# Kernel optimization log

Measured on AMD Instinct MI355X. Metric: run time of the kernel, lower is better.

## Reference

```python
import jax, jax.numpy as jnp
import numpy as np

D_MODEL = 1024
NUM_HEADS = 16
D_K = D_MODEL // NUM_HEADS


def setup_inputs() -> dict:
    key = jax.random.key(0)
    ks = jax.random.split(key, 9)
    s = 1.0 / np.sqrt(D_MODEL)
    x = jax.random.normal(ks[0], (2, 2048, D_MODEL), dtype=jnp.float32)
    mk = lambda k: jax.random.uniform(k, (D_MODEL, D_MODEL), jnp.float32, -s, s)
    mb = lambda k: jax.random.uniform(k, (D_MODEL,), jnp.float32, -s, s)
    return {
        "x": x,
        "Wq": mk(ks[1]), "bq": mb(ks[2]),
        "Wk": mk(ks[3]), "bk": mb(ks[4]),
        "Wv": mk(ks[5]), "bv": mb(ks[6]),
        "Wo": mk(ks[7]), "bo": mb(ks[8]),
    }


def _attn(x, Wq, bq, Wk, bk, Wv, bv, Wo, bo):
    B, S, _ = x.shape
    # torch Linear: y = x @ W.T + b; weights stored [out, in]
    def proj(W, b):
        y = jnp.einsum('bsd,ed->bse', x, W) + b
        return y.reshape(B, S, NUM_HEADS, D_K).transpose(0, 2, 1, 3)  # [B,H,S,Dk]
    Q = proj(Wq, bq)
    K = proj(Wk, bk)
    V = proj(Wv, bv)
    scale = 1.0 / np.sqrt(D_K).astype(np.float32)
    scores = jnp.einsum('bhqd,bhkd->bhqk', Q, K) * scale  # [B,H,S,S]
    # FAITHFUL to source: softmax over dim=1 (the HEAD axis), a quirk of the original code
    attn = jax.nn.softmax(scores, axis=1)
    context = jnp.einsum('bhqk,bhkd->bhqd', attn, V)  # [B,H,S,Dk]
    context = context.transpose(0, 2, 1, 3).reshape(B, S, D_MODEL)
    return jnp.einsum('bsd,ed->bse', context, Wo) + bo


def reference(x, Wq, bq, Wk, bk, Wv, bv, Wo, bo):
    return _attn(x, Wq, bq, Wk, bk, Wv, bv, Wo, bo)
```

## Files before the change

kernel.cpp:

```cpp
#include <hip/hip_runtime.h>


#define D_MODEL 1024
#define NH 16
#define DKH 64
#define SEQ 2048
#define NB 2
#define NTOK (NB * SEQ)
#define OSC 0.180336880f

typedef float f32x4 __attribute__((ext_vector_type(4)));
typedef short bf16x8 __attribute__((ext_vector_type(8)));

static __device__ __forceinline__ unsigned short f2bf(float x) {
    union { float f; unsigned int u; } c; c.f = x;
    unsigned int r = (c.u + 0x7FFFu + ((c.u >> 16) & 1u)) >> 16;
    return (unsigned short)r;
}
static __device__ __forceinline__ unsigned int pack2(float a, float b) {
    return (unsigned int)f2bf(a) | ((unsigned int)f2bf(b) << 16);
}
static __device__ __forceinline__ unsigned int pack2rn(float a, float b) {
    union { float f; unsigned int u; } ca, cb; ca.f = a; cb.f = b;
    return __builtin_amdgcn_perm(cb.u + 0x8000u, ca.u + 0x8000u, 0x07060302u);
}
static __device__ __forceinline__ unsigned int pack2tr(float a, float b) {
    union { float f; unsigned int u; } ca, cb; ca.f = a; cb.f = b;
    return __builtin_amdgcn_perm(cb.u, ca.u, 0x07060302u);
}
static __device__ __forceinline__ float bflo(unsigned int u) {
    union { unsigned int x; float f; } c; c.x = u << 16; return c.f;
}
static __device__ __forceinline__ float bfhi(unsigned int u) {
    union { unsigned int x; float f; } c; c.x = u & 0xFFFF0000u; return c.f;
}
static __device__ __forceinline__ f32x4 mfma16(uint4 a, uint4 b, f32x4 c) {
    return __builtin_amdgcn_mfma_f32_16x16x32_bf16(
        __builtin_bit_cast(bf16x8, a), __builtin_bit_cast(bf16x8, b), c, 0, 0, 0);
}
static __device__ __forceinline__ void gl_lds16(const unsigned short* g, unsigned short* l) {
    __builtin_amdgcn_global_load_lds(
        (const __attribute__((address_space(1))) unsigned int*)g,
        (__attribute__((address_space(3))) unsigned int*)l, 16, 0, 0);
}
static __device__ __forceinline__ int fsw(int row) {
    return (row & 7) ^ ((row >> 2) & 7);
}

__global__ __launch_bounds__(256) void cvt_k(const float* __restrict__ x,
                                             unsigned short* __restrict__ xb)
{
    size_t i = ((size_t)blockIdx.x * 256 + threadIdx.x) * 8;
    float4 a = *(const float4*)(x + i);
    float4 b = *(const float4*)(x + i + 4);
    uint4 p = { pack2(a.x, a.y), pack2(a.z, a.w), pack2(b.x, b.y), pack2(b.z, b.w) };
    *(uint4*)(xb + i) = p;
}

__global__ __launch_bounds__(256) void cvt_w3(
    const float* __restrict__ w0, const float* __restrict__ w1,
    const float* __restrict__ w2, unsigned short* __restrict__ outb)
{
    int sel = blockIdx.x >> 9;
    int blk = blockIdx.x & 511;
    const float* src = (sel == 0) ? w0 : (sel == 1) ? w1 : w2;
    size_t i = ((size_t)blk * 256 + threadIdx.x) * 8;
    float4 a = *(const float4*)(src + i);
    float4 b = *(const float4*)(src + i + 4);
    uint4 p = { pack2(a.x, a.y), pack2(a.z, a.w), pack2(b.x, b.y), pack2(b.z, b.w) };
    *(uint4*)(outb + (size_t)sel * D_MODEL * D_MODEL + i) = p;
}

__global__ __launch_bounds__(256) void gemm_qkv3(
    const unsigned short* __restrict__ A, const unsigned short* __restrict__ Wb3,
    const float* __restrict__ bq, const float* __restrict__ bk,
    const float* __restrict__ bv, unsigned short* __restrict__ Qh,
    unsigned short* __restrict__ Kh, unsigned short* __restrict__ Vt)
{
    __shared__ unsigned short lds[16384];
    unsigned short* lA = lds;
    unsigned short* lB = lds + 8192;
    const int tid = threadIdx.x;
    const int wv = tid >> 6, lane = tid & 63, quad = lane >> 4, lm = lane & 15;
    const int sel = blockIdx.x >> 3;
    const int m0 = blockIdx.y * 128, n0 = (blockIdx.x & 7) * 128;
    const int sub = lane >> 3, chl = (lane & 7) ^ sub;
    const unsigned short* Wb = Wb3 + (size_t)sel * D_MODEL * D_MODEL;
    const float* bias = (sel == 0) ? bq : (sel == 1) ? bk : bv;
    const float osc = (sel == 0) ? OSC : 1.0f;

    f32x4 acc[2][8] = {};

    for (int k0 = 0; k0 < D_MODEL; k0 += 64) {
        __syncthreads();
#pragma unroll
        for (int j = 0; j < 4; ++j) {
            int rbase = wv * 32 + j * 8;
            gl_lds16(A + (size_t)(m0 + rbase + sub) * D_MODEL + k0 + chl * 8,
                     &lA[rbase * 64]);
            gl_lds16(Wb + (size_t)(n0 + rbase + sub) * D_MODEL + k0 + chl * 8,
                     &lB[rbase * 64]);
        }
        __syncthreads();
#pragma unroll
        for (int ks = 0; ks < 2; ++ks) {
            uint4 af[2];
#pragma unroll
            for (int mt = 0; mt < 2; ++mt)
                af[mt] = *(const uint4*)&lA[(wv * 32 + mt * 16 + lm) * 64 +
                                            ((ks * 4 + quad) ^ (lm & 7)) * 8];
#pragma unroll
            for (int nt = 0; nt < 8; ++nt) {
                uint4 bf = *(const uint4*)&lB[(nt * 16 + lm) * 64 +
                                              ((ks * 4 + quad) ^ (lm & 7)) * 8];
                acc[0][nt] = mfma16(af[0], bf, acc[0][nt]);
                acc[1][nt] = mfma16(af[1], bf, acc[1][nt]);
            }
        }
    }

    if (sel < 2) {
        unsigned short* out = (sel == 0) ? Qh : Kh;
#pragma unroll
        for (int nt = 0; nt < 8; ++nt) {
            int n = n0 + nt * 16 + lm;
            float bvv = bias[n];
            int h = n >> 6, d = n & 63;
#pragma unroll
            for (int mt = 0; mt < 2; ++mt)
#pragma unroll
                for (int r = 0; r < 4; ++r) {
                    int m = m0 + wv * 32 + mt * 16 + quad * 4 + r;
                    int b = m >> 11, q = m & 2047;
                    out[((size_t)(b * NH + h) * SEQ + q) * DKH + d] =
                        f2bf((acc[mt][nt][r] + bvv) * osc);
                }
        }
    } else {
        __syncthreads();
        unsigned short* T = lds;
#pragma unroll
        for (int nt = 0; nt < 8; ++nt) {
            float bvv = bias[n0 + nt * 16 + lm];
            int nl = nt * 16 + lm;
#pragma unroll
            for (int mt = 0; mt < 2; ++mt) {
                int ml = wv * 32 + mt * 16 + quad * 4;
                uint2 p = { pack2rn(acc[mt][nt][0] + bvv, acc[mt][nt][1] + bvv),
                            pack2rn(acc[mt][nt][2] + bvv, acc[mt][nt][3] + bvv) };
                *(uint2*)&T[nl * 128 + ml] = p;
            }
        }
        __syncthreads();
        int row = tid >> 1, seg = tid & 1;
        int b = m0 >> 11, s0 = m0 & 2047;
        unsigned short* dst = Vt + ((size_t)(b * D_MODEL) + n0 + row) * SEQ + s0 + seg * 64;
        const unsigned short* src = &T[row * 128 + seg * 64];
#pragma unroll
        for (int i = 0; i < 8; ++i)
            *(uint4*)(dst + i * 8) = *(const uint4*)(src + i * 8);
    }
}

template <int KS>
__global__ __launch_bounds__(256) void psum(const unsigned short* __restrict__ OP,
                                            unsigned short* __restrict__ OPs)
{
    const size_t M = (size_t)NTOK * D_MODEL;
    size_t i = ((size_t)blockIdx.x * 256 + threadIdx.x) * 8;
    uint4 a = *(const uint4*)(OP + i);
    float lo0 = bflo(a.x), hi0 = bfhi(a.x), lo1 = bflo(a.y), hi1 = bfhi(a.y);
    float lo2 = bflo(a.z), hi2 = bfhi(a.z), lo3 = bflo(a.w), hi3 = bfhi(a.w);
#pragma unroll
    for (int p = 1; p < KS; ++p) {
        uint4 u = *(const uint4*)(OP + p * M + i);
        lo0 += bflo(u.x); hi0 += bfhi(u.x); lo1 += bflo(u.y); hi1 += bfhi(u.y);
        lo2 += bflo(u.z); hi2 += bfhi(u.z); lo3 += bflo(u.w); hi3 += bfhi(u.w);
    }
    uint4 o = { pack2(lo0, hi0), pack2(lo1, hi1), pack2(lo2, hi2), pack2(lo3, hi3) };
    *(uint4*)(OPs + i) = o;
}

__global__ __launch_bounds__(256) void gemm_osum1(
    const unsigned short* __restrict__ OPs, const unsigned short* __restrict__ WoB,
    const float* __restrict__ bias, float* __restrict__ out)
{
    __shared__ unsigned short lds[16384];
    unsigned short* lA = lds;
    unsigned short* lB = lds + 8192;
    const int tid = threadIdx.x;
    const int wv = tid >> 6, lane = tid & 63, quad = lane >> 4, lm = lane & 15;
    const int m0 = blockIdx.y * 128, n0 = blockIdx.x * 128;
    const int sub = lane >> 3, chl = (lane & 7) ^ sub;
    const int b = m0 >> 11, q0 = m0 & 2047;

    f32x4 acc[2][8] = {};

    for (int k0 = 0; k0 < D_MODEL; k0 += 64) {
        const int h = k0 >> 6;
        const unsigned short* Ab = OPs + ((size_t)(b * NH + h) * SEQ + q0) * DKH;
        __syncthreads();
#pragma unroll
        for (int j = 0; j < 4; ++j) {
            int rbase = wv * 32 + j * 8;
            gl_lds16(Ab + (size_t)(rbase + sub) * DKH + chl * 8, &lA[rbase * 64]);
            gl_lds16(WoB + (size_t)(n0 + rbase + sub) * D_MODEL + k0 + chl * 8,
                     &lB[rbase * 64]);
        }
        __syncthreads();
#pragma unroll
        for (int ks = 0; ks < 2; ++ks) {
            uint4 af[2];
#pragma unroll
            for (int mt = 0; mt < 2; ++mt)
                af[mt] = *(const uint4*)&lA[(wv * 32 + mt * 16 + lm) * 64 +
                                            ((ks * 4 + quad) ^ (lm & 7)) * 8];
#pragma unroll
            for (int nt = 0; nt < 8; ++nt) {
                uint4 bf = *(const uint4*)&lB[(nt * 16 + lm) * 64 +
                                              ((ks * 4 + quad) ^ (lm & 7)) * 8];
                acc[0][nt] = mfma16(af[0], bf, acc[0][nt]);
                acc[1][nt] = mfma16(af[1], bf, acc[1][nt]);
            }
        }
    }
#pragma unroll
    for (int nt = 0; nt < 8; ++nt) {
        int n = n0 + nt * 16 + lm;
        float bv = bias[n];
#pragma unroll
        for (int mt = 0; mt < 2; ++mt)
#pragma unroll
            for (int r = 0; r < 4; ++r) {
                int m = m0 + wv * 32 + mt * 16 + quad * 4 + r;
                out[(size_t)m * D_MODEL + n] = acc[mt][nt][r] + bv;
            }
    }
}

__global__ __launch_bounds__(256) void zker2(
    const unsigned short* __restrict__ Qh, const unsigned short* __restrict__ Kh,
    unsigned short* __restrict__ rz)
{
    __shared__ unsigned short lK[2][128 * 64];
    const int tid = threadIdx.x;
    const int wv = tid >> 6, lane = tid & 63, quad = lane >> 4, lm = lane & 15;
    const int lid = blockIdx.x;
    const int xcd = lid & 7, slot = lid >> 3;
    const int qb = slot & 15, col = xcd * 4 + (slot >> 4);
    const int b = col >> 4, kb = col & 15;
    const int q0 = qb * 128, k0 = kb * 128;
    const int srow = tid >> 3, sc = tid & 7;

    f32x4 z[2][8] = {};

    auto stagek = [&](int buf, int hh) {
        const size_t kbase = ((size_t)(b * NH + hh) * SEQ + k0) * DKH;
#pragma unroll
        for (int j = 0; j < 4; ++j) {
            int row = j * 32 + srow;
            int g = sc ^ fsw(row);
            gl_lds16(Kh + kbase + (size_t)row * 64 + g * 8,
                     &lK[buf][(j * 32 + wv * 8) * 64]);
        }
    };
    auto loadq = [&](uint4 (&bqr)[2][2], int hh) {
#pragma unroll
        for (int qs = 0; qs < 2; ++qs) {
            const unsigned short* qp = Qh +
                ((size_t)(b * NH + hh) * SEQ + q0 + wv * 32 + qs * 16 + lm) * DKH + quad * 8;
            bqr[qs][0] = *(const uint4*)qp;
            bqr[qs][1] = *(const uint4*)(qp + 32);
        }
    };

    uint4 bq[2][2];
    stagek(0, 0);
    loadq(bq, 0);
    __syncthreads();

    for (int h = 0; h < NH; ++h) {
        const int cur = h & 1;
        uint4 bqn[2][2];
        if (h + 1 < NH) {
            stagek(cur ^ 1, h + 1);
            loadq(bqn, h + 1);
        }
        const unsigned short* cK = lK[cur];
#pragma unroll
        for (int kt = 0; kt < 8; ++kt) {
            int krow = kt * 16 + lm;
            uint4 a0 = *(const uint4*)&cK[krow * 64 + ((quad) ^ fsw(krow)) * 8];
            uint4 a1 = *(const uint4*)&cK[krow * 64 + ((4 + quad) ^ fsw(krow)) * 8];
#pragma unroll
            for (int qs = 0; qs < 2; ++qs) {
                f32x4 sf = {0.f, 0.f, 0.f, 0.f};
                __builtin_amdgcn_s_setprio(1);
                sf = mfma16(a0, bq[qs][0], sf);
                sf = mfma16(a1, bq[qs][1], sf);
                __builtin_amdgcn_s_setprio(0);
#pragma unroll
                for (int r = 0; r < 4; ++r)
                    z[qs][kt][r] += __builtin_amdgcn_exp2f(sf[r]);
            }
        }
        __syncthreads();
        if (h + 1 < NH) {
#pragma unroll
            for (int qs = 0; qs < 2; ++qs) {
                bq[qs][0] = bqn[qs][0];
                bq[qs][1] = bqn[qs][1];
            }
        }
    }
#pragma unroll
    for (int qs = 0; qs < 2; ++qs) {
        int q = q0 + wv * 32 + qs * 16 + lm;
#pragma unroll
        for (int kt = 0; kt < 8; ++kt) {
            int k = k0 + kt * 16 + quad * 4;
            float l0 = __builtin_amdgcn_logf(z[qs][kt][0]);
            float l1 = __builtin_amdgcn_logf(z[qs][kt][1]);
            float l2 = __builtin_amdgcn_logf(z[qs][kt][2]);
            float l3 = __builtin_amdgcn_logf(z[qs][kt][3]);
            uint2 st = { pack2rn(-l0, -l1), pack2rn(-l2, -l3) };
            *(uint2*)(rz + (size_t)(b * SEQ + q) * SEQ + k) = st;
        }
    }
}

template <int KS>
__global__ __launch_bounds__(256) void attn4(
    const unsigned short* __restrict__ Qh, const unsigned short* __restrict__ Kh,
    const unsigned short* __restrict__ Vt, const unsigned short* __restrict__ rz,
    unsigned short* __restrict__ OP)
{
    __shared__ unsigned short lK[2][64 * 64];
    __shared__ unsigned short lV[2][64 * 64];
    const int tid = threadIdx.x;
    const int wv = tid >> 6, lane = tid & 63, quad = lane >> 4, lm = lane & 15;
    const int lid = blockIdx.x;
    const int xcd = lid & 7, slot = lid >> 3;
    const int qb = slot & 15;
    const int combo = xcd * (4 * KS) + (slot >> 4);
    const int bh = combo / KS, ksl = combo % KS;
    const int b = bh >> 4, h = bh & 15;
    const int q0 = qb * 128;
    const int NIT = (SEQ / KS) / 64;
    const int kbeg = ksl * (SEQ / KS);
    const int q0w = q0 + wv * 32;
    const size_t hb = (size_t)(b * NH + h) * SEQ;
    const int srow = tid >> 3, sc = tid & 7;

    uint4 qf[2][2];
#pragma unroll
    for (int qs = 0; qs < 2; ++qs)
#pragma unroll
        for (int ks = 0; ks < 2; ++ks)
            qf[qs][ks] = *(const uint4*)(Qh + (hb + q0w + qs * 16 + lm) * DKH +
                                         ks * 32 + quad * 8);

    auto stage = [&](int buf, int kb2) {
#pragma unroll
        for (int j = 0; j < 2; ++j) {
            int row = j * 32 + srow;
            int g = sc ^ fsw(row);
            gl_lds16(Kh + (hb + kb2 + row) * DKH + g * 8,
                     &lK[buf][(j * 32 + wv * 8) * 64]);
        }
#pragma unroll
        for (int j = 0; j < 2; ++j) {
            int row = j * 32 + srow;
            int g = sc ^ fsw(row);
            gl_lds16(Vt + ((size_t)(b * D_MODEL) + h * DKH + row) * SEQ + kb2 + g * 8,
                     &lV[buf][(j * 32 + wv * 8) * 64]);
        }
    };
    auto loadrv = [&](uint4 (&r)[2][2], int kb2) {
#pragma unroll
        for (int qs = 0; qs < 2; ++qs)
#pragma unroll
            for (int gr = 0; gr < 2; ++gr)
                r[gr][qs] = *(const uint4*)(rz +
                    (size_t)(b * SEQ + q0w + qs * 16 + lm) * SEQ +
                    kb2 + gr * 32 + quad * 8);
    };

    const int perm = ((lm >> 2) * 8) + (lm & 3);
    f32x4 oa[4][2] = {};

    uint4 rv[2][2];
    stage(0, kbeg);
    loadrv(rv, kbeg);
    __syncthreads();

    for (int kt = 0; kt < NIT; ++kt) {
        const int cur = kt & 1;
        const int kbase = kbeg + kt * 64;
        uint4 rvn[2][2];
        if (kt + 1 < NIT) {
            stage(cur ^ 1, kbase + 64);
            loadrv(rvn, kbase + 64);
        }
        const unsigned short* cK = lK[cur];
        const unsigned short* cV = lV[cur];

#pragma unroll
        for (int gr = 0; gr < 2; ++gr) {
            f32x4 sf[2][2];
#pragma unroll
            for (int qs = 0; qs < 2; ++qs) {
                uint4 rq = rv[gr][qs];
                sf[0][qs][0] = bflo(rq.x); sf[0][qs][1] = bfhi(rq.x);
                sf[0][qs][2] = bflo(rq.y); sf[0][qs][3] = bfhi(rq.y);
                sf[1][qs][0] = bflo(rq.z); sf[1][qs][1] = bfhi(rq.z);
                sf[1][qs][2] = bflo(rq.w); sf[1][qs][3] = bfhi(rq.w);
            }
            __builtin_amdgcn_s_setprio(1);
#pragma unroll
            for (int sel = 0; sel < 2; ++sel) {
                int key = gr * 32 + perm + sel * 4;
#pragma unroll
                for (int ks = 0; ks < 2; ++ks) {
                    uint4 kfv = *(const uint4*)&cK[key * 64 +
                                                   ((ks * 4 + quad) ^ fsw(key)) * 8];
                    sf[sel][0] = mfma16(kfv, qf[0][ks], sf[sel][0]);
                    sf[sel][1] = mfma16(kfv, qf[1][ks], sf[sel][1]);
                }
            }
            __builtin_amdgcn_s_setprio(0);
            uint4 pk[2];
#pragma unroll
            for (int qs = 0; qs < 2; ++qs) {
                float p00 = __builtin_amdgcn_exp2f(sf[0][qs][0]);
                float p01 = __builtin_amdgcn_exp2f(sf[0][qs][1]);
                float p02 = __builtin_amdgcn_exp2f(sf[0][qs][2]);
                float p03 = __builtin_amdgcn_exp2f(sf[0][qs][3]);
                float p10 = __builtin_amdgcn_exp2f(sf[1][qs][0]);
                float p11 = __builtin_amdgcn_exp2f(sf[1][qs][1]);
                float p12 = __builtin_amdgcn_exp2f(sf[1][qs][2]);
                float p13 = __builtin_amdgcn_exp2f(sf[1][qs][3]);
                pk[qs].x = pack2tr(p00, p01);
                pk[qs].y = pack2tr(p02, p03);
                pk[qs].z = pack2tr(p10, p11);
                pk[qs].w = pack2tr(p12, p13);
            }
            __builtin_amdgcn_s_setprio(1);
#pragma unroll
            for (int ct = 0; ct < 4; ++ct) {
                int vrow = ct * 16 + lm;
                uint4 vfv = *(const uint4*)&cV[vrow * 64 +
                                               ((gr * 4 + quad) ^ fsw(vrow)) * 8];
                oa[ct][0] = mfma16(vfv, pk[0], oa[ct][0]);
                oa[ct][1] = mfma16(vfv, pk[1], oa[ct][1]);
            }
            __builtin_amdgcn_s_setprio(0);
        }
        __syncthreads();
        if (kt + 1 < NIT) {
#pragma unroll
            for (int a = 0; a < 2; ++a)
#pragma unroll
                for (int c = 0; c < 2; ++c)
                    rv[a][c] = rvn[a][c];
        }
    }

    unsigned short* op = OP + (size_t)ksl * NTOK * D_MODEL;
#pragma unroll
    for (int ct = 0; ct < 4; ++ct)
#pragma unroll
        for (int qs = 0; qs < 2; ++qs) {
            uint2 st = { pack2rn(oa[ct][qs][0], oa[ct][qs][1]),
                         pack2rn(oa[ct][qs][2], oa[ct][qs][3]) };
            *(uint2*)(op + (hb + q0w + qs * 16 + lm) * DKH + ct * 16 + quad * 4) = st;
        }
}

extern "C" void kernel_launch(void* const* d_in, const int* in_sizes, int n_in,
                              void* d_out, int out_size, void* d_ws, size_t ws_size,
                              hipStream_t stream)
{
    const float* x  = (const float*)d_in[0];
    const float* Wq = (const float*)d_in[1];
    const float* bq = (const float*)d_in[2];
    const float* Wk = (const float*)d_in[3];
    const float* bk = (const float*)d_in[4];
    const float* Wv = (const float*)d_in[5];
    const float* bv = (const float*)d_in[6];
    const float* Wo = (const float*)d_in[7];
    const float* bo = (const float*)d_in[8];
    float* out = (float*)d_out;

    const size_t M  = (size_t)NTOK * D_MODEL;
    const size_t RZ = (size_t)NB * SEQ * SEQ;
    unsigned short* ws = (unsigned short*)d_ws;
    unsigned short* rzb = ws;
    unsigned short* xb  = ws;
    unsigned short* Qh  = ws + RZ;
    unsigned short* Kh  = Qh + M;
    unsigned short* Vt  = Kh + M;
    unsigned short* OP  = Vt + M;
    unsigned short* Wb3 = OP;
    unsigned short* OPs = Qh;
    unsigned short* WoB = rzb;

    const size_t need4 = (RZ + 3 * M + 4 * M) * sizeof(unsigned short);
    const size_t need2 = (RZ + 3 * M + 2 * M) * sizeof(unsigned short);
    const int KS = (ws_size >= need4) ? 4 : (ws_size >= need2) ? 2 : 1;

    cvt_k<<<2048, 256, 0, stream>>>(x, xb);
    cvt_w3<<<1536, 256, 0, stream>>>(Wq, Wk, Wv, Wb3);
    gemm_qkv3<<<dim3(24, 32), 256, 0, stream>>>(xb, Wb3, bq, bk, bv, Qh, Kh, Vt);
    zker2<<<512, 256, 0, stream>>>(Qh, Kh, rzb);
    if (KS == 4)      attn4<4><<<2048, 256, 0, stream>>>(Qh, Kh, Vt, rzb, OP);
    else if (KS == 2) attn4<2><<<1024, 256, 0, stream>>>(Qh, Kh, Vt, rzb, OP);
    else              attn4<1><<<512, 256, 0, stream>>>(Qh, Kh, Vt, rzb, OP);
    cvt_k<<<512, 256, 0, stream>>>(Wo, WoB);
    if (KS == 4)      psum<4><<<2048, 256, 0, stream>>>(OP, OPs);
    else if (KS == 2) psum<2><<<2048, 256, 0, stream>>>(OP, OPs);
    else              OPs = OP;
    gemm_osum1<<<dim3(8, 32), 256, 0, stream>>>(OPs, WoB, bo, out);
}
```

Measured before the change: 272.2 us.

## Shrink output GEMM tile to 128x64 and drop attention double-buffering

```diff
diff --git a/kernel.cpp b/kernel.cpp
--- a/kernel.cpp
+++ b/kernel.cpp
@@ -181,20 +181,21 @@
     *(uint4*)(OPs + i) = o;
 }
 
-__global__ __launch_bounds__(256) void gemm_osum1(
+__global__ __launch_bounds__(256) void gemm_osum2(
     const unsigned short* __restrict__ OPs, const unsigned short* __restrict__ WoB,
     const float* __restrict__ bias, float* __restrict__ out)
 {
-    __shared__ unsigned short lds[16384];
+    __shared__ unsigned short lds[12288];
     unsigned short* lA = lds;
     unsigned short* lB = lds + 8192;
     const int tid = threadIdx.x;
     const int wv = tid >> 6, lane = tid & 63, quad = lane >> 4, lm = lane & 15;
-    const int m0 = blockIdx.y * 128, n0 = blockIdx.x * 128;
+    const int wm = wv >> 1, wn = wv & 1;
+    const int m0 = blockIdx.y * 128, n0 = blockIdx.x * 64;
     const int sub = lane >> 3, chl = (lane & 7) ^ sub;
     const int b = m0 >> 11, q0 = m0 & 2047;
 
-    f32x4 acc[2][8] = {};
+    f32x4 acc[4][2] = {};
 
     for (int k0 = 0; k0 < D_MODEL; k0 += 64) {
         const int h = k0 >> 6;
@@ -204,35 +205,40 @@
         for (int j = 0; j < 4; ++j) {
             int rbase = wv * 32 + j * 8;
             gl_lds16(Ab + (size_t)(rbase + sub) * DKH + chl * 8, &lA[rbase * 64]);
+        }
+#pragma unroll
+        for (int j = 0; j < 2; ++j) {
+            int rbase = wv * 16 + j * 8;
             gl_lds16(WoB + (size_t)(n0 + rbase + sub) * D_MODEL + k0 + chl * 8,
                      &lB[rbase * 64]);
         }
         __syncthreads();
 #pragma unroll
         for (int ks = 0; ks < 2; ++ks) {
-            uint4 af[2];
-#pragma unroll
-            for (int mt = 0; mt < 2; ++mt)
-                af[mt] = *(const uint4*)&lA[(wv * 32 + mt * 16 + lm) * 64 +
+            uint4 af[4];
+#pragma unroll
+            for (int mt = 0; mt < 4; ++mt)
+                af[mt] = *(const uint4*)&lA[(wm * 64 + mt * 16 + lm) * 64 +
                                             ((ks * 4 + quad) ^ (lm & 7)) * 8];
 #pragma unroll
-            for (int nt = 0; nt < 8; ++nt) {
-                uint4 bf = *(const uint4*)&lB[(nt * 16 + lm) * 64 +
+            for (int nt = 0; nt < 2; ++nt) {
+                uint4 bf = *(const uint4*)&lB[(wn * 32 + nt * 16 + lm) * 64 +
                                               ((ks * 4 + quad) ^ (lm & 7)) * 8];
-                acc[0][nt] = mfma16(af[0], bf, acc[0][nt]);
-                acc[1][nt] = mfma16(af[1], bf, acc[1][nt]);
-            }
-        }
-    }
-#pragma unroll
-    for (int nt = 0; nt < 8; ++nt) {
-        int n = n0 + nt * 16 + lm;
+#pragma unroll
+                for (int mt = 0; mt < 4; ++mt)
+                    acc[mt][nt] = mfma16(af[mt], bf, acc[mt][nt]);
+            }
+        }
+    }
+#pragma unroll
+    for (int nt = 0; nt < 2; ++nt) {
+        int n = n0 + wn * 32 + nt * 16 + lm;
         float bv = bias[n];
 #pragma unroll
-        for (int mt = 0; mt < 2; ++mt)
+        for (int mt = 0; mt < 4; ++mt)
 #pragma unroll
             for (int r = 0; r < 4; ++r) {
-                int m = m0 + wv * 32 + mt * 16 + quad * 4 + r;
+                int m = m0 + wm * 64 + mt * 16 + quad * 4 + r;
                 out[(size_t)m * D_MODEL + n] = acc[mt][nt][r] + bv;
             }
     }
@@ -335,8 +341,8 @@
     const unsigned short* __restrict__ Vt, const unsigned short* __restrict__ rz,
     unsigned short* __restrict__ OP)
 {
-    __shared__ unsigned short lK[2][64 * 64];
-    __shared__ unsigned short lV[2][64 * 64];
+    __shared__ unsigned short lK[64 * 64];
+    __shared__ unsigned short lV[64 * 64];
     const int tid = threadIdx.x;
     const int wv = tid >> 6, lane = tid & 63, quad = lane >> 4, lm = lane & 15;
     const int lid = blockIdx.x;
@@ -360,50 +366,35 @@
             qf[qs][ks] = *(const uint4*)(Qh + (hb + q0w + qs * 16 + lm) * DKH +
                                          ks * 32 + quad * 8);
 
-    auto stage = [&](int buf, int kb2) {
+    const int perm = ((lm >> 2) * 8) + (lm & 3);
+    f32x4 oa[4][2] = {};
+
+    for (int kt = 0; kt < NIT; ++kt) {
+        const int kbase = kbeg + kt * 64;
+        __syncthreads();
 #pragma unroll
         for (int j = 0; j < 2; ++j) {
             int row = j * 32 + srow;
             int g = sc ^ fsw(row);
-            gl_lds16(Kh + (hb + kb2 + row) * DKH + g * 8,
-                     &lK[buf][(j * 32 + wv * 8) * 64]);
+            gl_lds16(Kh + (hb + kbase + row) * DKH + g * 8,
+                     &lK[(j * 32 + wv * 8) * 64]);
         }
 #pragma unroll
         for (int j = 0; j < 2; ++j) {
             int row = j * 32 + srow;
             int g = sc ^ fsw(row);
-            gl_lds16(Vt + ((size_t)(b * D_MODEL) + h * DKH + row) * SEQ + kb2 + g * 8,
-                     &lV[buf][(j * 32 + wv * 8) * 64]);
-        }
-    };
-    auto loadrv = [&](uint4 (&r)[2][2], int kb2) {
+            gl_lds16(Vt + ((size_t)(b * D_MODEL) + h * DKH + row) * SEQ + kbase + g * 8,
+                     &lV[(j * 32 + wv * 8) * 64]);
+        }
+        uint4 rv[2][2];
 #pragma unroll
         for (int qs = 0; qs < 2; ++qs)
 #pragma unroll
             for (int gr = 0; gr < 2; ++gr)
-                r[gr][qs] = *(const uint4*)(rz +
+                rv[gr][qs] = *(const uint4*)(rz +
                     (size_t)(b * SEQ + q0w + qs * 16 + lm) * SEQ +
-                    kb2 + gr * 32 + quad * 8);
-    };
-
-    const int perm = ((lm >> 2) * 8) + (lm & 3);
-    f32x4 oa[4][2] = {};
-
-    uint4 rv[2][2];
-    stage(0, kbeg);
-    loadrv(rv, kbeg);
-    __syncthreads();
-
-    for (int kt = 0; kt < NIT; ++kt) {
-        const int cur = kt & 1;
-        const int kbase = kbeg + kt * 64;
-        uint4 rvn[2][2];
-        if (kt + 1 < NIT) {
-            stage(cur ^ 1, kbase + 64);
-            loadrv(rvn, kbase + 64);
-        }
-        const unsigned short* cK = lK[cur];
-        const unsigned short* cV = lV[cur];
+                    kbase + gr * 32 + quad * 8);
+        __syncthreads();
 
 #pragma unroll
         for (int gr = 0; gr < 2; ++gr) {
@@ -422,7 +413,7 @@
                 int key = gr * 32 + perm + sel * 4;
 #pragma unroll
                 for (int ks = 0; ks < 2; ++ks) {
-                    uint4 kfv = *(const uint4*)&cK[key * 64 +
+                    uint4 kfv = *(const uint4*)&lK[key * 64 +
                                                    ((ks * 4 + quad) ^ fsw(key)) * 8];
                     sf[sel][0] = mfma16(kfv, qf[0][ks], sf[sel][0]);
                     sf[sel][1] = mfma16(kfv, qf[1][ks], sf[sel][1]);
@@ -449,20 +440,12 @@
 #pragma unroll
             for (int ct = 0; ct < 4; ++ct) {
                 int vrow = ct * 16 + lm;
-                uint4 vfv = *(const uint4*)&cV[vrow * 64 +
+                uint4 vfv = *(const uint4*)&lV[vrow * 64 +
                                                ((gr * 4 + quad) ^ fsw(vrow)) * 8];
                 oa[ct][0] = mfma16(vfv, pk[0], oa[ct][0]);
                 oa[ct][1] = mfma16(vfv, pk[1], oa[ct][1]);
             }
             __builtin_amdgcn_s_setprio(0);
-        }
-        __syncthreads();
-        if (kt + 1 < NIT) {
-#pragma unroll
-            for (int a = 0; a < 2; ++a)
-#pragma unroll
-                for (int c = 0; c < 2; ++c)
-                    rv[a][c] = rvn[a][c];
         }
     }
 
@@ -520,5 +503,5 @@
     if (KS == 4)      psum<4><<<2048, 256, 0, stream>>>(OP, OPs);
     else if (KS == 2) psum<2><<<2048, 256, 0, stream>>>(OP, OPs);
     else              OPs = OP;
-    gemm_osum1<<<dim3(8, 32), 256, 0, stream>>>(OPs, WoB, bo, out);
-}
+    gemm_osum2<<<dim3(16, 32), 256, 0, stream>>>(OPs, WoB, bo, out);
+}
```

New measurement: 263.3 us. 3.3% less time.
